# Kernel optimization log

Hardware: AMD Instinct MI355X
Metric: run time of the kernel (lower is better)

Reference implementation:

```python
import jax, jax.numpy as jnp
import numpy as np

B, TQ, TY = 8, 400, 400
Q_DIM, Y_DIM, ATT_DIM = 256, 256, 128


def setup_inputs() -> dict:
    key = jax.random.key(0)
    ks = jax.random.split(key, 9)
    s_q = 1.0 / np.sqrt(Q_DIM)
    s_y = 1.0 / np.sqrt(Y_DIM)
    s_a = 1.0 / np.sqrt(ATT_DIM)
    return {
        "query": jax.random.normal(ks[0], (B, TQ, Q_DIM), jnp.float32),
        "y": jax.random.normal(ks[1], (B, TY, Y_DIM), jnp.float32),
        "Wq_w": jax.random.uniform(ks[2], (ATT_DIM, Q_DIM), jnp.float32, -s_q, s_q),
        "Wq_b": jax.random.uniform(ks[3], (ATT_DIM,), jnp.float32, -s_q, s_q),
        "Wy_w": jax.random.uniform(ks[4], (ATT_DIM, Y_DIM), jnp.float32, -s_y, s_y),
        "Wy_b": jax.random.uniform(ks[5], (ATT_DIM,), jnp.float32, -s_y, s_y),
        "v_w": jax.random.uniform(ks[6], (1, ATT_DIM), jnp.float32, -s_a, s_a),
        "v_b": jax.random.uniform(ks[7], (1,), jnp.float32, -s_a, s_a),
        "n_wins_y": jax.random.randint(ks[8], (B,), TY // 2, TY + 1, jnp.int64 if jax.config.jax_enable_x64 else jnp.int32),
    }


def reference(query, y, Wq_w, Wq_b, Wy_w, Wy_b, v_w, v_b, n_wins_y):
    # Bahdanau scores: tanh(Wq(q)[:,None,:,:] + Wy(y)[:,:,None,:]) -> [B,Ty,Tq,A]
    q_proj = jnp.einsum('bqd,ad->bqa', query, Wq_w) + Wq_b      # [B,Tq,A]
    y_proj = jnp.einsum('btd,ad->bta', y, Wy_w) + Wy_b          # [B,Ty,A]
    h = jnp.tanh(q_proj[:, None, :, :] + y_proj[:, :, None, :])  # [B,Ty,Tq,A]
    att = jnp.einsum('btqa,a->btq', h, v_w[0]) + v_b[0]          # [B,Ty,Tq]
    att = jnp.transpose(att, (0, 2, 1))                          # [B,Tq,Ty]
    # mask invalid y windows (dim 2 = Ty), then softmax over Ty
    mask = jnp.arange(att.shape[2])[None, None, :] < n_wins_y[:, None, None]
    att = jnp.where(mask, att, -jnp.inf)
    att = jax.nn.softmax(att, axis=2)
    # soft attention apply: bmm(att, y) -> [B,Tq,y_dim]
    return jnp.einsum('bqt,btd->bqd', att, y)
```

## Files before the change

kernel.cpp:

```cpp
#include <hip/hip_runtime.h>


#define LOG2E 1.4426950408889634f
#define TANH_SCALE 2.8853900817779268f

constexpr int TQn = 400, TYn = 400, AD = 128, DD = 256;
constexpr int QT = 8;
constexpr int QBLOCKS = TQn / QT;
constexpr int SSTR = 65;
constexpr int PSTR = 409;

__global__ __launch_bounds__(128) void transpose_kernel(
    const float* __restrict__ Wq, const float* __restrict__ Wy,
    float4* __restrict__ WTq, float4* __restrict__ WTy)
{
    const int k4 = blockIdx.x & 63;
    const bool isq = blockIdx.x < 64;
    const float4* src = reinterpret_cast<const float4*>(isq ? Wq : Wy);
    float4* dst = isq ? WTq : WTy;
    const int a = threadIdx.x;
    dst[k4 * 128 + a] = src[a * 64 + k4];
}

__global__ __launch_bounds__(256, 4) void proj_kernel(
    const float* __restrict__ qin, const float* __restrict__ yin,
    const float4* __restrict__ WTq, const float* __restrict__ bq,
    const float4* __restrict__ WTy, const float* __restrict__ by,
    float* __restrict__ Eq, float* __restrict__ Ey)
{
    const int blk = blockIdx.x;
    const bool is_q = blk < 400;
    const int row0 = (is_q ? blk : blk - 400) * 8;
    const float* in   = (is_q ? qin : yin) + (size_t)row0 * DD;
    const float4* wt  = is_q ? WTq : WTy;
    const float* bias = is_q ? bq : by;
    float* outp = (is_q ? Eq : Ey) + (size_t)row0 * AD;

    __shared__ float lin[8 * DD];
    __shared__ float red[8][AD];
    {
        const float4* in4 = reinterpret_cast<const float4*>(in);
        float4* l4s = reinterpret_cast<float4*>(lin);
        l4s[threadIdx.x]       = in4[threadIdx.x];
        l4s[threadIdx.x + 256] = in4[threadIdx.x + 256];
    }
    __syncthreads();

    const int a = threadIdx.x & 127;
    const int h = threadIdx.x >> 7;
    float acc[8] = {0.f,0.f,0.f,0.f,0.f,0.f,0.f,0.f};
    const float4* l4 = reinterpret_cast<const float4*>(lin);
    #pragma unroll 8
    for (int i = 0; i < 32; ++i) {
        const int k4 = h * 32 + i;
        float4 w4 = wt[k4 * 128 + a];
        #pragma unroll
        for (int r = 0; r < 8; ++r) {
            float4 v = l4[r * 64 + k4];
            acc[r] = fmaf(w4.x, v.x, acc[r]);
            acc[r] = fmaf(w4.y, v.y, acc[r]);
            acc[r] = fmaf(w4.z, v.z, acc[r]);
            acc[r] = fmaf(w4.w, v.w, acc[r]);
        }
    }
    if (h) {
        #pragma unroll
        for (int r = 0; r < 8; ++r) red[r][a] = acc[r];
    }
    __syncthreads();
    if (!h) {
        const float bb = bias[a];
        #pragma unroll
        for (int r = 0; r < 8; ++r)
            outp[(size_t)r * AD + a] =
                __builtin_amdgcn_exp2f((acc[r] + red[r][a] + bb) * TANH_SCALE);
    }
}

__global__ __launch_bounds__(512, 4) void fused_kernel(
    const float* __restrict__ y,
    const float* __restrict__ Eq,
    const float* __restrict__ Ey,
    const float* __restrict__ vw,
    const int*  __restrict__ nwins,
    float* __restrict__ out)
{
    __shared__ float4 s_eq4[QT * 32];
    __shared__ float4 s_v4[32];
    __shared__ float4 s_big[32 * SSTR];
    __shared__ float  s_p[QT][PSTR];

    const int b  = blockIdx.x / QBLOCKS;
    const int q0 = (blockIdx.x % QBLOCKS) * QT;
    const int tid = threadIdx.x;
    const int wave = tid >> 6;
    const int lane = tid & 63;
    const int n = nwins[b];
    const float NEG_INF = -__builtin_inff();

    const float4* eyb = reinterpret_cast<const float4*>(Ey);
    const float4* yb  = reinterpret_cast<const float4*>(y) + (size_t)(b * TYn) * 64;

    const int pcol = tid & 31;
    const int prow = tid >> 5;

    float4 p0, p1, p2, p3;
    {
        const size_t base = (size_t)(b * TYn) * 32 + pcol;
        p0 = eyb[base + (size_t)(prow +  0) * 32];
        p1 = eyb[base + (size_t)(prow + 16) * 32];
        p2 = eyb[base + (size_t)(prow + 32) * 32];
        p3 = eyb[base + (size_t)(prow + 48) * 32];
    }
    if (tid < QT * 32) {
        s_eq4[tid] = reinterpret_cast<const float4*>(Eq + (size_t)(b * TQn + q0) * AD)[tid];
    } else if (tid < QT * 32 + 32) {
        float4 v = reinterpret_cast<const float4*>(vw)[tid - QT * 32];
        s_v4[tid - QT * 32] = make_float4(-2.f * v.x, -2.f * v.y, -2.f * v.z, -2.f * v.w);
    }

    float sc[7];
    #pragma unroll
    for (int j = 0; j < 7; ++j) sc[j] = NEG_INF;
    const int ntile = (n + 63) >> 6;

    #pragma unroll
    for (int i = 0; i < 7; ++i) {
        if (i < ntile) {
            __syncthreads();
            s_big[pcol * SSTR + prow +  0] = p0;
            s_big[pcol * SSTR + prow + 16] = p1;
            s_big[pcol * SSTR + prow + 32] = p2;
            s_big[pcol * SSTR + prow + 48] = p3;
            if (i + 1 < ntile) {
                const int t0n = (i + 1) * 64;
                const size_t base = (size_t)(b * TYn) * 32 + pcol;
                int r0 = min(t0n + prow +  0, TYn - 1);
                int r1 = min(t0n + prow + 16, TYn - 1);
                int r2 = min(t0n + prow + 32, TYn - 1);
                int r3 = min(t0n + prow + 48, TYn - 1);
                p0 = eyb[base + (size_t)r0 * 32];
                p1 = eyb[base + (size_t)r1 * 32];
                p2 = eyb[base + (size_t)r2 * 32];
                p3 = eyb[base + (size_t)r3 * 32];
            }
            __syncthreads();
            float ac0 = 0.f, ac1 = 0.f, ac2 = 0.f, ac3 = 0.f;
            const float4* qrow = s_eq4 + wave * 32;
            #pragma unroll 8
            for (int a4 = 0; a4 < 32; ++a4) {
                float4 yv = s_big[a4 * SSTR + lane];
                float4 qv = qrow[a4];
                float4 vv = s_v4[a4];
                float a0 = fmaf(qv.x, yv.x, 1.f);
                float a1 = fmaf(qv.y, yv.y, 1.f);
                float a2 = fmaf(qv.z, yv.z, 1.f);
                float a3 = fmaf(qv.w, yv.w, 1.f);
                float p01 = a0 * a1, p23 = a2 * a3;
                float R = __builtin_amdgcn_rcpf(p01 * p23);
                float u = p23 * R, w = p01 * R;
                ac0 = fmaf(vv.x, a1 * u, ac0);
                ac1 = fmaf(vv.y, a0 * u, ac1);
                ac2 = fmaf(vv.z, a3 * w, ac2);
                ac3 = fmaf(vv.w, a2 * w, ac3);
            }
            sc[i] = (ac0 + ac1) + (ac2 + ac3);
        }
    }
    __syncthreads();

    const int scol = tid & 63, srow0 = tid >> 6;
    float4 g0 = yb[(size_t)(srow0    ) * 64 + scol];
    float4 g1 = yb[(size_t)(srow0 + 8) * 64 + scol];

    #pragma unroll
    for (int j = 0; j < 7; ++j) {
        int t = j * 64 + lane;
        if (t >= n) sc[j] = NEG_INF;
    }
    float m = sc[0];
    #pragma unroll
    for (int j = 1; j < 7; ++j) m = fmaxf(m, sc[j]);
    #pragma unroll
    for (int off = 32; off >= 1; off >>= 1) m = fmaxf(m, __shfl_xor(m, off, 64));
    float l = 0.f;
    #pragma unroll
    for (int j = 0; j < 7; ++j) {
        float pv = __builtin_amdgcn_exp2f((sc[j] - m) * LOG2E);
        sc[j] = pv;
        l += pv;
    }
    #pragma unroll
    for (int off = 32; off >= 1; off >>= 1) l += __shfl_xor(l, off, 64);
    const float inv = 1.0f / l;
    #pragma unroll
    for (int j = 0; j < 7; ++j) {
        const int t = j * 64 + lane;
        if (t < TYn) s_p[wave][t] = sc[j] * inv;
    }

    const int q  = lane >> 3;
    const int d4 = (wave << 3) | (lane & 7);
    float4 acc = {0.f, 0.f, 0.f, 0.f};
    const int nta = (n + 15) >> 4;
    for (int i = 0; i < nta; ++i) {
        float4* buf = s_big + (i & 1) * 1024;
        buf[(srow0    ) * 64 + scol] = g0;
        buf[(srow0 + 8) * 64 + scol] = g1;
        if (i + 1 < nta) {
            const int t0n = (i + 1) * 16;
            g0 = yb[(size_t)(t0n + srow0    ) * 64 + scol];
            g1 = yb[(size_t)(t0n + srow0 + 8) * 64 + scol];
        }
        __syncthreads();
        const int tb = i * 16;
        #pragma unroll
        for (int ttl = 0; ttl < 16; ++ttl) {
            const float  pt = s_p[q][tb + ttl];
            const float4 yv = buf[ttl * 64 + d4];
            acc.x = fmaf(pt, yv.x, acc.x);
            acc.y = fmaf(pt, yv.y, acc.y);
            acc.z = fmaf(pt, yv.z, acc.z);
            acc.w = fmaf(pt, yv.w, acc.w);
        }
    }
    reinterpret_cast<float4*>(out)[(size_t)(b * TQn + q0 + q) * 64 + d4] = acc;
}

extern "C" void kernel_launch(void* const* d_in, const int* in_sizes, int n_in,
                              void* d_out, int out_size, void* d_ws, size_t ws_size,
                              hipStream_t stream) {
    const float* query = (const float*)d_in[0];
    const float* y     = (const float*)d_in[1];
    const float* Wq_w  = (const float*)d_in[2];
    const float* Wq_b  = (const float*)d_in[3];
    const float* Wy_w  = (const float*)d_in[4];
    const float* Wy_b  = (const float*)d_in[5];
    const float* v_w   = (const float*)d_in[6];
    const int* nw      = (const int*)d_in[8];
    float* out = (float*)d_out;

    float4* WTq = (float4*)d_ws;
    float4* WTy = WTq + 64 * 128;
    float*  Eq  = (float*)(WTy + 64 * 128);
    float*  Ey  = Eq + (size_t)8 * TQn * AD;

    transpose_kernel<<<128, 128, 0, stream>>>(Wq_w, Wy_w, WTq, WTy);
    proj_kernel<<<800, 256, 0, stream>>>(query, y, WTq, Wq_b, WTy, Wy_b, Eq, Ey);
    fused_kernel<<<8 * QBLOCKS, 512, 0, stream>>>(y, Eq, Ey, v_w, nw, out);
}
```

Baseline: 67.66 us.

## Restructure projection and fused attention kernels with register reuse and direct global reads

The projection kernel now gives each thread 8 full rows and caches 8 weight float4s in registers. It drops the shared-memory input staging and the cross-half reduction, and runs half as many blocks with 16 rows each. The fused kernel moves from 512 to 256 threads, and each wave computes scores for two query rows so every Ey tile load from shared memory is reused. Eq and v rows are read straight from global memory rather than staged. The attention-apply stage no longer stages y in shared memory; it reads y directly from global/L2 with float4 probability vectors, and each thread produces two output float4s. This trades shared-memory traffic and barriers for more global/cache loads and fewer waves per block.

Result: slower. 109.5 us (+61.9%).

```diff
diff --git a/kernel.cpp b/kernel.cpp
--- a/kernel.cpp
+++ b/kernel.cpp
@@ -8,7 +8,7 @@
 constexpr int QT = 8;
 constexpr int QBLOCKS = TQn / QT;
 constexpr int SSTR = 65;
-constexpr int PSTR = 409;
+constexpr int PROW = 404;
 
 __global__ __launch_bounds__(128) void transpose_kernel(
     const float* __restrict__ Wq, const float* __restrict__ Wy,
@@ -22,62 +22,49 @@
     dst[k4 * 128 + a] = src[a * 64 + k4];
 }
 
-__global__ __launch_bounds__(256, 4) void proj_kernel(
+__global__ __launch_bounds__(256) void proj_kernel(
     const float* __restrict__ qin, const float* __restrict__ yin,
     const float4* __restrict__ WTq, const float* __restrict__ bq,
     const float4* __restrict__ WTy, const float* __restrict__ by,
     float* __restrict__ Eq, float* __restrict__ Ey)
 {
     const int blk = blockIdx.x;
-    const bool is_q = blk < 400;
-    const int row0 = (is_q ? blk : blk - 400) * 8;
-    const float* in   = (is_q ? qin : yin) + (size_t)row0 * DD;
+    const bool is_q = blk < 200;
+    const int row0 = (is_q ? blk : blk - 200) * 16;
+    const int a  = threadIdx.x & 127;
+    const int rh = threadIdx.x >> 7;
+    const float4* in4 = reinterpret_cast<const float4*>(
+        (is_q ? qin : yin) + (size_t)(row0 + rh * 8) * DD);
     const float4* wt  = is_q ? WTq : WTy;
     const float* bias = is_q ? bq : by;
-    float* outp = (is_q ? Eq : Ey) + (size_t)row0 * AD;
-
-    __shared__ float lin[8 * DD];
-    __shared__ float red[8][AD];
-    {
-        const float4* in4 = reinterpret_cast<const float4*>(in);
-        float4* l4s = reinterpret_cast<float4*>(lin);
-        l4s[threadIdx.x]       = in4[threadIdx.x];
-        l4s[threadIdx.x + 256] = in4[threadIdx.x + 256];
-    }
-    __syncthreads();
-
-    const int a = threadIdx.x & 127;
-    const int h = threadIdx.x >> 7;
+    float* outp = (is_q ? Eq : Ey) + (size_t)(row0 + rh * 8) * AD;
+
     float acc[8] = {0.f,0.f,0.f,0.f,0.f,0.f,0.f,0.f};
-    const float4* l4 = reinterpret_cast<const float4*>(lin);
-    #pragma unroll 8
-    for (int i = 0; i < 32; ++i) {
-        const int k4 = h * 32 + i;
-        float4 w4 = wt[k4 * 128 + a];
+    for (int c = 0; c < 8; ++c) {
+        float4 wreg[8];
+        #pragma unroll
+        for (int j = 0; j < 8; ++j)
+            wreg[j] = wt[(c * 8 + j) * 128 + a];
         #pragma unroll
         for (int r = 0; r < 8; ++r) {
-            float4 v = l4[r * 64 + k4];
-            acc[r] = fmaf(w4.x, v.x, acc[r]);
-            acc[r] = fmaf(w4.y, v.y, acc[r]);
-            acc[r] = fmaf(w4.z, v.z, acc[r]);
-            acc[r] = fmaf(w4.w, v.w, acc[r]);
+            #pragma unroll
+            for (int j = 0; j < 8; ++j) {
+                float4 v = in4[r * 64 + c * 8 + j];
+                acc[r] = fmaf(wreg[j].x, v.x, acc[r]);
+                acc[r] = fmaf(wreg[j].y, v.y, acc[r]);
+                acc[r] = fmaf(wreg[j].z, v.z, acc[r]);
+                acc[r] = fmaf(wreg[j].w, v.w, acc[r]);
+            }
         }
     }
-    if (h) {
-        #pragma unroll
-        for (int r = 0; r < 8; ++r) red[r][a] = acc[r];
-    }
-    __syncthreads();
-    if (!h) {
-        const float bb = bias[a];
-        #pragma unroll
-        for (int r = 0; r < 8; ++r)
-            outp[(size_t)r * AD + a] =
-                __builtin_amdgcn_exp2f((acc[r] + red[r][a] + bb) * TANH_SCALE);
-    }
-}
-
-__global__ __launch_bounds__(512, 4) void fused_kernel(
+    const float bb = bias[a];
+    #pragma unroll
+    for (int r = 0; r < 8; ++r)
+        outp[(size_t)r * AD + a] =
+            __builtin_amdgcn_exp2f((acc[r] + bb) * TANH_SCALE);
+}
+
+__global__ __launch_bounds__(256) void fused_kernel(
     const float* __restrict__ y,
     const float* __restrict__ Eq,
     const float* __restrict__ Ey,
@@ -85,10 +72,8 @@
     const int*  __restrict__ nwins,
     float* __restrict__ out)
 {
-    __shared__ float4 s_eq4[QT * 32];
-    __shared__ float4 s_v4[32];
-    __shared__ float4 s_big[32 * SSTR];
-    __shared__ float  s_p[QT][PSTR];
+    __shared__ float4 s_ey[32 * SSTR];
+    __shared__ __align__(16) float s_p[QT][PROW];
 
     const int b  = blockIdx.x / QBLOCKS;
     const int q0 = (blockIdx.x % QBLOCKS) * QT;
@@ -99,132 +84,143 @@
     const float NEG_INF = -__builtin_inff();
 
     const float4* eyb = reinterpret_cast<const float4*>(Ey);
-    const float4* yb  = reinterpret_cast<const float4*>(y) + (size_t)(b * TYn) * 64;
-
-    const int pcol = tid & 31;
-    const int prow = tid >> 5;
-
-    float4 p0, p1, p2, p3;
-    {
-        const size_t base = (size_t)(b * TYn) * 32 + pcol;
-        p0 = eyb[base + (size_t)(prow +  0) * 32];
-        p1 = eyb[base + (size_t)(prow + 16) * 32];
-        p2 = eyb[base + (size_t)(prow + 32) * 32];
-        p3 = eyb[base + (size_t)(prow + 48) * 32];
-    }
-    if (tid < QT * 32) {
-        s_eq4[tid] = reinterpret_cast<const float4*>(Eq + (size_t)(b * TQn + q0) * AD)[tid];
-    } else if (tid < QT * 32 + 32) {
-        float4 v = reinterpret_cast<const float4*>(vw)[tid - QT * 32];
-        s_v4[tid - QT * 32] = make_float4(-2.f * v.x, -2.f * v.y, -2.f * v.z, -2.f * v.w);
-    }
-
-    float sc[7];
-    #pragma unroll
-    for (int j = 0; j < 7; ++j) sc[j] = NEG_INF;
+    const float4* yb4 = reinterpret_cast<const float4*>(y) + (size_t)(b * TYn) * 64;
+    const float4* vw4 = reinterpret_cast<const float4*>(vw);
+    const float4* eqlo = reinterpret_cast<const float4*>(Eq)
+                       + (size_t)(b * TQn + q0 + wave) * 32;
+    const float4* eqhi = eqlo + 4 * 32;
+
+    const int scol = tid & 31;
+    const int srow = tid >> 5;
+
+    float sc_lo[7], sc_hi[7];
+    #pragma unroll
+    for (int j = 0; j < 7; ++j) { sc_lo[j] = NEG_INF; sc_hi[j] = NEG_INF; }
     const int ntile = (n + 63) >> 6;
 
     #pragma unroll
     for (int i = 0; i < 7; ++i) {
         if (i < ntile) {
+            const int t0 = i * 64;
             __syncthreads();
-            s_big[pcol * SSTR + prow +  0] = p0;
-            s_big[pcol * SSTR + prow + 16] = p1;
-            s_big[pcol * SSTR + prow + 32] = p2;
-            s_big[pcol * SSTR + prow + 48] = p3;
-            if (i + 1 < ntile) {
-                const int t0n = (i + 1) * 64;
-                const size_t base = (size_t)(b * TYn) * 32 + pcol;
-                int r0 = min(t0n + prow +  0, TYn - 1);
-                int r1 = min(t0n + prow + 16, TYn - 1);
-                int r2 = min(t0n + prow + 32, TYn - 1);
-                int r3 = min(t0n + prow + 48, TYn - 1);
-                p0 = eyb[base + (size_t)r0 * 32];
-                p1 = eyb[base + (size_t)r1 * 32];
-                p2 = eyb[base + (size_t)r2 * 32];
-                p3 = eyb[base + (size_t)r3 * 32];
+            #pragma unroll
+            for (int k = 0; k < 8; ++k) {
+                const int r = min(t0 + srow + 8 * k, TYn - 1);
+                s_ey[scol * SSTR + srow + 8 * k] =
+                    eyb[(size_t)(b * TYn + r) * 32 + scol];
             }
             __syncthreads();
-            float ac0 = 0.f, ac1 = 0.f, ac2 = 0.f, ac3 = 0.f;
-            const float4* qrow = s_eq4 + wave * 32;
+            float al0 = 0.f, al1 = 0.f, al2 = 0.f, al3 = 0.f;
+            float ah0 = 0.f, ah1 = 0.f, ah2 = 0.f, ah3 = 0.f;
             #pragma unroll 8
             for (int a4 = 0; a4 < 32; ++a4) {
-                float4 yv = s_big[a4 * SSTR + lane];
-                float4 qv = qrow[a4];
-                float4 vv = s_v4[a4];
-                float a0 = fmaf(qv.x, yv.x, 1.f);
-                float a1 = fmaf(qv.y, yv.y, 1.f);
-                float a2 = fmaf(qv.z, yv.z, 1.f);
-                float a3 = fmaf(qv.w, yv.w, 1.f);
-                float p01 = a0 * a1, p23 = a2 * a3;
-                float R = __builtin_amdgcn_rcpf(p01 * p23);
-                float u = p23 * R, w = p01 * R;
-                ac0 = fmaf(vv.x, a1 * u, ac0);
-                ac1 = fmaf(vv.y, a0 * u, ac1);
-                ac2 = fmaf(vv.z, a3 * w, ac2);
-                ac3 = fmaf(vv.w, a2 * w, ac3);
+                const float4 yv = s_ey[a4 * SSTR + lane];
+                const float4 vv = vw4[a4];
+                {
+                    const float4 qv = eqlo[a4];
+                    float a0 = fmaf(qv.x, yv.x, 1.f);
+                    float a1 = fmaf(qv.y, yv.y, 1.f);
+                    float a2 = fmaf(qv.z, yv.z, 1.f);
+                    float a3 = fmaf(qv.w, yv.w, 1.f);
+                    float p01 = a0 * a1, p23 = a2 * a3;
+                    float R = __builtin_amdgcn_rcpf(p01 * p23);
+                    float t1 = p23 * R, t2 = p01 * R;
+                    float u = t1 + t1, w2 = t2 + t2;
+                    al0 = fmaf(vv.x, -(a1 * u),  al0);
+                    al1 = fmaf(vv.y, -(a0 * u),  al1);
+                    al2 = fmaf(vv.z, -(a3 * w2), al2);
+                    al3 = fmaf(vv.w, -(a2 * w2), al3);
+                }
+                {
+                    const float4 qv = eqhi[a4];
+                    float a0 = fmaf(qv.x, yv.x, 1.f);
+                    float a1 = fmaf(qv.y, yv.y, 1.f);
+                    float a2 = fmaf(qv.z, yv.z, 1.f);
+                    float a3 = fmaf(qv.w, yv.w, 1.f);
+                    float p01 = a0 * a1, p23 = a2 * a3;
+                    float R = __builtin_amdgcn_rcpf(p01 * p23);
+                    float t1 = p23 * R, t2 = p01 * R;
+                    float u = t1 + t1, w2 = t2 + t2;
+                    ah0 = fmaf(vv.x, -(a1 * u),  ah0);
+                    ah1 = fmaf(vv.y, -(a0 * u),  ah1);
+                    ah2 = fmaf(vv.z, -(a3 * w2), ah2);
+                    ah3 = fmaf(vv.w, -(a2 * w2), ah3);
+                }
             }
-            sc[i] = (ac0 + ac1) + (ac2 + ac3);
+            sc_lo[i] = (al0 + al1) + (al2 + al3);
+            sc_hi[i] = (ah0 + ah1) + (ah2 + ah3);
         }
     }
-    __syncthreads();
-
-    const int scol = tid & 63, srow0 = tid >> 6;
-    float4 g0 = yb[(size_t)(srow0    ) * 64 + scol];
-    float4 g1 = yb[(size_t)(srow0 + 8) * 64 + scol];
-
-    #pragma unroll
-    for (int j = 0; j < 7; ++j) {
-        int t = j * 64 + lane;
-        if (t >= n) sc[j] = NEG_INF;
-    }
-    float m = sc[0];
-    #pragma unroll
-    for (int j = 1; j < 7; ++j) m = fmaxf(m, sc[j]);
-    #pragma unroll
-    for (int off = 32; off >= 1; off >>= 1) m = fmaxf(m, __shfl_xor(m, off, 64));
-    float l = 0.f;
-    #pragma unroll
-    for (int j = 0; j < 7; ++j) {
-        float pv = __builtin_amdgcn_exp2f((sc[j] - m) * LOG2E);
-        sc[j] = pv;
-        l += pv;
-    }
-    #pragma unroll
-    for (int off = 32; off >= 1; off >>= 1) l += __shfl_xor(l, off, 64);
-    const float inv = 1.0f / l;
+
     #pragma unroll
     for (int j = 0; j < 7; ++j) {
         const int t = j * 64 + lane;
-        if (t < TYn) s_p[wave][t] = sc[j] * inv;
-    }
-
-    const int q  = lane >> 3;
-    const int d4 = (wave << 3) | (lane & 7);
-    float4 acc = {0.f, 0.f, 0.f, 0.f};
-    const int nta = (n + 15) >> 4;
-    for (int i = 0; i < nta; ++i) {
-        float4* buf = s_big + (i & 1) * 1024;
-        buf[(srow0    ) * 64 + scol] = g0;
-        buf[(srow0 + 8) * 64 + scol] = g1;
-        if (i + 1 < nta) {
-            const int t0n = (i + 1) * 16;
-            g0 = yb[(size_t)(t0n + srow0    ) * 64 + scol];
-            g1 = yb[(size_t)(t0n + srow0 + 8) * 64 + scol];
+        if (t >= n) { sc_lo[j] = NEG_INF; sc_hi[j] = NEG_INF; }
+    }
+    float mlo = sc_lo[0], mhi = sc_hi[0];
+    #pragma unroll
+    for (int j = 1; j < 7; ++j) { mlo = fmaxf(mlo, sc_lo[j]); mhi = fmaxf(mhi, sc_hi[j]); }
+    #pragma unroll
+    for (int off = 32; off >= 1; off >>= 1) {
+        mlo = fmaxf(mlo, __shfl_xor(mlo, off, 64));
+        mhi = fmaxf(mhi, __shfl_xor(mhi, off, 64));
+    }
+    float llo = 0.f, lhi = 0.f;
+    #pragma unroll
+    for (int j = 0; j < 7; ++j) {
+        sc_lo[j] = __builtin_amdgcn_exp2f((sc_lo[j] - mlo) * LOG2E);
+        sc_hi[j] = __builtin_amdgcn_exp2f((sc_hi[j] - mhi) * LOG2E);
+        llo += sc_lo[j]; lhi += sc_hi[j];
+    }
+    #pragma unroll
+    for (int off = 32; off >= 1; off >>= 1) {
+        llo += __shfl_xor(llo, off, 64);
+        lhi += __shfl_xor(lhi, off, 64);
+    }
+    const float invlo = 1.0f / llo, invhi = 1.0f / lhi;
+    #pragma unroll
+    for (int j = 0; j < 7; ++j) {
+        const int t = j * 64 + lane;
+        if (t < TYn) {
+            s_p[wave][t]     = sc_lo[j] * invlo;
+            s_p[wave + 4][t] = sc_hi[j] * invhi;
         }
-        __syncthreads();
-        const int tb = i * 16;
-        #pragma unroll
-        for (int ttl = 0; ttl < 16; ++ttl) {
-            const float  pt = s_p[q][tb + ttl];
-            const float4 yv = buf[ttl * 64 + d4];
-            acc.x = fmaf(pt, yv.x, acc.x);
-            acc.y = fmaf(pt, yv.y, acc.y);
-            acc.z = fmaf(pt, yv.z, acc.z);
-            acc.w = fmaf(pt, yv.w, acc.w);
-        }
-    }
-    reinterpret_cast<float4*>(out)[(size_t)(b * TQn + q0 + q) * 64 + d4] = acc;
+    }
+    __syncthreads();
+
+    const int q   = lane >> 3;
+    const int d4a = (wave << 3) | (lane & 7);
+    const int d4b = d4a + 32;
+    const float4* prow4 = reinterpret_cast<const float4*>(&s_p[q][0]);
+    float4 acca = {0.f,0.f,0.f,0.f}, accb = {0.f,0.f,0.f,0.f};
+    const int n4q = (n + 3) >> 2;
+    for (int tq = 0; tq < n4q; ++tq) {
+        const float4 pv = prow4[tq];
+        const float4* yr = yb4 + (size_t)(tq * 4) * 64;
+        const float4 A0 = yr[d4a],        B0 = yr[d4b];
+        const float4 A1 = yr[64  + d4a],  B1 = yr[64  + d4b];
+        const float4 A2 = yr[128 + d4a],  B2 = yr[128 + d4b];
+        const float4 A3 = yr[192 + d4a],  B3 = yr[192 + d4b];
+        acca.x = fmaf(pv.x, A0.x, acca.x); acca.y = fmaf(pv.x, A0.y, acca.y);
+        acca.z = fmaf(pv.x, A0.z, acca.z); acca.w = fmaf(pv.x, A0.w, acca.w);
+        accb.x = fmaf(pv.x, B0.x, accb.x); accb.y = fmaf(pv.x, B0.y, accb.y);
+        accb.z = fmaf(pv.x, B0.z, accb.z); accb.w = fmaf(pv.x, B0.w, accb.w);
+        acca.x = fmaf(pv.y, A1.x, acca.x); acca.y = fmaf(pv.y, A1.y, acca.y);
+        acca.z = fmaf(pv.y, A1.z, acca.z); acca.w = fmaf(pv.y, A1.w, acca.w);
+        accb.x = fmaf(pv.y, B1.x, accb.x); accb.y = fmaf(pv.y, B1.y, accb.y);
+        accb.z = fmaf(pv.y, B1.z, accb.z); accb.w = fmaf(pv.y, B1.w, accb.w);
+        acca.x = fmaf(pv.z, A2.x, acca.x); acca.y = fmaf(pv.z, A2.y, acca.y);
+        acca.z = fmaf(pv.z, A2.z, acca.z); acca.w = fmaf(pv.z, A2.w, acca.w);
+        accb.x = fmaf(pv.z, B2.x, accb.x); accb.y = fmaf(pv.z, B2.y, accb.y);
+        accb.z = fmaf(pv.z, B2.z, accb.z); accb.w = fmaf(pv.z, B2.w, accb.w);
+        acca.x = fmaf(pv.w, A3.x, acca.x); acca.y = fmaf(pv.w, A3.y, acca.y);
+        acca.z = fmaf(pv.w, A3.z, acca.z); acca.w = fmaf(pv.w, A3.w, acca.w);
+        accb.x = fmaf(pv.w, B3.x, accb.x); accb.y = fmaf(pv.w, B3.y, accb.y);
+        accb.z = fmaf(pv.w, B3.z, accb.z); accb.w = fmaf(pv.w, B3.w, accb.w);
+    }
+    float4* o4 = reinterpret_cast<float4*>(out) + (size_t)(b * TQn + q0 + q) * 64;
+    o4[d4a] = acca;
+    o4[d4b] = accb;
 }
 
 extern "C" void kernel_launch(void* const* d_in, const int* in_sizes, int n_in,
@@ -246,6 +242,6 @@
     float*  Ey  = Eq + (size_t)8 * TQn * AD;
 
     transpose_kernel<<<128, 128, 0, stream>>>(Wq_w, Wy_w, WTq, WTy);
-    proj_kernel<<<800, 256, 0, stream>>>(query, y, WTq, Wq_b, WTy, Wy_b, Eq, Ey);
-    fused_kernel<<<8 * QBLOCKS, 512, 0, stream>>>(y, Eq, Ey, v_w, nw, out);
-}
+    proj_kernel<<<400, 256, 0, stream>>>(query, y, WTq, Wq_b, WTy, Wy_b, Eq, Ey);
+    fused_kernel<<<8 * QBLOCKS, 256, 0, stream>>>(y, Eq, Ey, v_w, nw, out);
+}
```
